# Optimization experiments

Measured on AMD Instinct MI355X. Metric: run time of the kernel, lower is better.

## Reference

```python
import jax, jax.numpy as jnp
import numpy as np

N_CHUNKS = 4 * 28  # hardcoded 112 chunks in the original; chunk sizes are equal when N % 112 == 0


def setup_inputs() -> dict:
    key = jax.random.key(0)
    k1, k2, k3 = jax.random.split(key, 3)
    b, d, h, w = 8, 512, 28, 28  # N = b*h*w = 6272, divisible by 112
    x = jax.random.normal(k1, (b, d, h, w), dtype=jnp.float32)
    p_mu = jax.random.normal(k2, (b * h * w, d), dtype=jnp.float32)
    p_logvar = jax.random.normal(k3, (b * h * w, d), dtype=jnp.float32)
    return {"x": x, "p_mu": p_mu, "p_logvar": p_logvar}


def _club_loss(x, p_mu, p_logvar):
    # (b, d, h, w) -> (N, d) with N = b*h*w
    b, d, h, w = x.shape
    flat_x = jnp.transpose(x, (0, 2, 3, 1)).reshape(-1, d)  # (N, d)

    inv_ev = jnp.exp(-p_logvar)  # (N, d)

    # positive[i] = -0.5 * sum_d (x_i - mu_i)^2 / exp(logvar_i)
    positive = -0.5 * jnp.sum(jnp.square(flat_x - p_mu) * inv_ev, axis=-1)  # (N,)

    # negative[i] = -0.5 * mean_j sum_d (x_j - mu_i)^2 / exp(logvar_i)
    # Expand the square so the j-contraction becomes GEMMs (no (N,N,d) intermediate):
    #   D[i,j] = <x_j^2, inv_ev_i> - 2 <x_j, mu_i * inv_ev_i> + <mu_i^2, inv_ev_i>
    x2 = jnp.square(flat_x)                                   # (N, d)
    term_x2 = jnp.einsum('id,jd->ij', inv_ev, x2)             # (N_i, N_j)
    term_cross = jnp.einsum('id,jd->ij', p_mu * inv_ev, flat_x)
    term_mu2 = jnp.sum(jnp.square(p_mu) * inv_ev, axis=-1, keepdims=True)  # (N_i, 1)
    D = term_x2 - 2.0 * term_cross + term_mu2                 # (N_i, N_j)
    negative = -0.5 * jnp.mean(D, axis=1)                     # (N,)

    # Original averages each of the 112 equal-size chunks then averages the
    # chunk means, which equals the global mean for equal chunk sizes.
    return jnp.mean(positive - negative)


def reference(x, p_mu, p_logvar):
    return _club_loss(x, p_mu, p_logvar)
```

## Files before the change

### kernel.cpp

```cpp
#include <hip/hip_runtime.h>


#define Dd   512
#define HWs  784
#define Nn   6272
#define LSx  260
#define NBLK 392


__global__ __launch_bounds__(256) void club_all(
    const float* __restrict__ x, const float* __restrict__ p_mu,
    const float* __restrict__ p_lv, float* __restrict__ ws,
    float* __restrict__ out)
{
    __shared__ __align__(16) float smem[2 * 16 * LSx];
    __shared__ float sbuf[16];
    __shared__ int lastFlag;

    const int t   = threadIdx.x;
    const int j   = blockIdx.x;
    const int b   = j / 49;
    const int ht  = j % 49;
    const int hw0 = ht * 16;
    const int r0  = b * HWs + hw0;
    const int rep = j & 7;

    const int dx = t >> 2, g = t & 3;
    const float* xb0 = x + ((size_t)(b * Dd + dx) * HWs + hw0 + 4 * g);
    const float4 A0 = *(const float4*)(xb0);
    const float4 A1 = *(const float4*)(xb0 +  64 * HWs);
    const float4 A2 = *(const float4*)(xb0 + 128 * HWs);
    const float4 A3 = *(const float4*)(xb0 + 192 * HWs);
    const float* xb1 = xb0 + 256 * HWs;
    const float4 B0 = *(const float4*)(xb1);
    const float4 B1 = *(const float4*)(xb1 +  64 * HWs);
    const float4 B2 = *(const float4*)(xb1 + 128 * HWs);
    const float4 B3 = *(const float4*)(xb1 + 192 * HWs);

    const size_t mb0 = (size_t)(r0 + (t >> 6)) * Dd + 4 * (t & 63);
    const float4 M00 = *(const float4*)(p_mu + mb0);
    const float4 M01 = *(const float4*)(p_mu + mb0 + 2048);
    const float4 M02 = *(const float4*)(p_mu + mb0 + 4096);
    const float4 M03 = *(const float4*)(p_mu + mb0 + 6144);
    const float4 L00 = *(const float4*)(p_lv + mb0);
    const float4 L01 = *(const float4*)(p_lv + mb0 + 2048);
    const float4 L02 = *(const float4*)(p_lv + mb0 + 4096);
    const float4 L03 = *(const float4*)(p_lv + mb0 + 6144);

#define XST(V, HALF, K) do {                                           \
        const int c_ = dx + 64 * (K);                                  \
        float* s_ = smem + (HALF) * 16 * LSx + (4 * g) * LSx + c_;     \
        s_[0 * LSx] = (V).x; s_[1 * LSx] = (V).y;                      \
        s_[2 * LSx] = (V).z; s_[3 * LSx] = (V).w;                      \
    } while (0)
    XST(A0, 0, 0); XST(A1, 0, 1); XST(A2, 0, 2); XST(A3, 0, 3);
    XST(B0, 1, 0); XST(B1, 1, 1); XST(B2, 1, 2); XST(B3, 1, 3);
#undef XST

    const size_t mb1 = mb0 + 256;
    const float4 M10 = *(const float4*)(p_mu + mb1);
    const float4 M11 = *(const float4*)(p_mu + mb1 + 2048);
    const float4 M12 = *(const float4*)(p_mu + mb1 + 4096);
    const float4 M13 = *(const float4*)(p_mu + mb1 + 6144);
    const float4 L10 = *(const float4*)(p_lv + mb1);
    const float4 L11 = *(const float4*)(p_lv + mb1 + 2048);
    const float4 L12 = *(const float4*)(p_lv + mb1 + 4096);
    const float4 L13 = *(const float4*)(p_lv + mb1 + 6144);

    __syncthreads();

    const int cc = 4 * (t & 63);
    const int rb = t >> 6;
    float4 aI0 = {0,0,0,0}, aM0 = {0,0,0,0}, sX0 = {0,0,0,0}, s20 = {0,0,0,0};
    float4 aI1 = {0,0,0,0}, aM1 = {0,0,0,0}, sX1 = {0,0,0,0}, s21 = {0,0,0,0};
    float aP = 0.f, aM2 = 0.f;

#define ACC1(XV, MU, LV, F, AI, AM, SX, S2) do {                       \
        const float iev = __expf(-(LV).F);                             \
        const float dd  = (XV).F - (MU).F;                             \
        aP += dd * dd * iev;                                           \
        (AI).F += iev;                                                 \
        const float mi = (MU).F * iev;                                 \
        (AM).F += mi; aM2 += (MU).F * mi;                              \
        (SX).F += (XV).F; (S2).F += (XV).F * (XV).F;                   \
    } while (0)
#define ACCROW(HALF, K, MU, LV, AI, AM, SX, S2) do {                   \
        const float4 xv = *(const float4*)&smem[(HALF)*16*LSx + (rb + 4*(K))*LSx + cc]; \
        ACC1(xv, MU, LV, x, AI, AM, SX, S2);                           \
        ACC1(xv, MU, LV, y, AI, AM, SX, S2);                           \
        ACC1(xv, MU, LV, z, AI, AM, SX, S2);                           \
        ACC1(xv, MU, LV, w, AI, AM, SX, S2);                           \
    } while (0)
    ACCROW(0, 0, M00, L00, aI0, aM0, sX0, s20);
    ACCROW(0, 1, M01, L01, aI0, aM0, sX0, s20);
    ACCROW(0, 2, M02, L02, aI0, aM0, sX0, s20);
    ACCROW(0, 3, M03, L03, aI0, aM0, sX0, s20);
    ACCROW(1, 0, M10, L10, aI1, aM1, sX1, s21);
    ACCROW(1, 1, M11, L11, aI1, aM1, sX1, s21);
    ACCROW(1, 2, M12, L12, aI1, aM1, sX1, s21);
    ACCROW(1, 3, M13, L13, aI1, aM1, sX1, s21);
#undef ACCROW
#undef ACC1

    float4* red4 = (float4*)smem;
    float4 rI0, rM0, rX0, r20, rI1, rM1, rX1, r21;
#define COLRED(SRC, DST) do {                                          \
        __syncthreads();                                               \
        red4[t] = (SRC);                                               \
        __syncthreads();                                               \
        if (t < 128) { float4 o = red4[t + 128];                       \
            red4[t].x += o.x; red4[t].y += o.y;                        \
            red4[t].z += o.z; red4[t].w += o.w; }                      \
        __syncthreads();                                               \
        if (t < 64) { float4 a = red4[t], o = red4[t + 64];            \
            (DST).x = a.x + o.x; (DST).y = a.y + o.y;                  \
            (DST).z = a.z + o.z; (DST).w = a.w + o.w; }                \
    } while (0)
    COLRED(aI0, rI0); COLRED(aM0, rM0); COLRED(sX0, rX0); COLRED(s20, r20);
    COLRED(aI1, rI1); COLRED(aM1, rM1); COLRED(sX1, rX1); COLRED(s21, r21);
#undef COLRED

#pragma unroll
    for (int off = 32; off > 0; off >>= 1) {
        aP  += __shfl_down(aP,  off);
        aM2 += __shfl_down(aM2, off);
    }
    __syncthreads();
    if ((t & 63) == 0) { sbuf[t >> 6] = aP; sbuf[8 + (t >> 6)] = aM2; }
    __syncthreads();

    if (t < 64) {
#define ATOM4(OFF, C, V) do {                                          \
        float* p_ = ws + (OFF) + rep * Dd + (C);                       \
        atomicAdd(p_ + 0, (V).x); atomicAdd(p_ + 1, (V).y);            \
        atomicAdd(p_ + 2, (V).z); atomicAdd(p_ + 3, (V).w);            \
    } while (0)
        ATOM4(0,     4 * t,       rI0); ATOM4(0,     256 + 4 * t, rI1);
        ATOM4(4096,  4 * t,       rM0); ATOM4(4096,  256 + 4 * t, rM1);
        ATOM4(8192,  4 * t,       rX0); ATOM4(8192,  256 + 4 * t, rX1);
        ATOM4(12288, 4 * t,       r20); ATOM4(12288, 256 + 4 * t, r21);
#undef ATOM4
    }
    if (t == 0) {
        double* wd = (double*)((char*)ws + 65536);
        atomicAdd(wd + rep,     (double)(sbuf[0] + sbuf[1] + sbuf[2] + sbuf[3]));
        atomicAdd(wd + 8 + rep, (double)(sbuf[8] + sbuf[9] + sbuf[10] + sbuf[11]));
    }

    if (t == 0) {
        __threadfence();
        unsigned* ctr = (unsigned*)((char*)ws + 65664);
        lastFlag = (atomicAdd(ctr, 1u) == NBLK - 1);
    }
    __syncthreads();
    if (!lastFlag) return;

    __threadfence();
    double* redd = (double*)smem;
    double dc = 0.0;
#pragma unroll
    for (int half = 0; half < 2; ++half) {
        const int c = t + 256 * half;
        double sI = 0.0, sM = 0.0, sX = 0.0, s2 = 0.0;
#pragma unroll
        for (int r = 0; r < 8; ++r) {
            sI += (double)__hip_atomic_load(ws +         r * Dd + c, __ATOMIC_RELAXED, __HIP_MEMORY_SCOPE_AGENT);
            sM += (double)__hip_atomic_load(ws +  4096 + r * Dd + c, __ATOMIC_RELAXED, __HIP_MEMORY_SCOPE_AGENT);
            sX += (double)__hip_atomic_load(ws +  8192 + r * Dd + c, __ATOMIC_RELAXED, __HIP_MEMORY_SCOPE_AGENT);
            s2 += (double)__hip_atomic_load(ws + 12288 + r * Dd + c, __ATOMIC_RELAXED, __HIP_MEMORY_SCOPE_AGENT);
        }
        dc += s2 * sI - 2.0 * sX * sM;
    }
    redd[t] = dc; __syncthreads();
    for (int s = 128; s > 0; s >>= 1) {
        if (t < s) redd[t] += redd[t + s];
        __syncthreads();
    }
    if (t == 0) {
        double* wd = (double*)((char*)ws + 65536);
        double P = 0.0, M2 = 0.0;
#pragma unroll
        for (int r = 0; r < 8; ++r) {
            P  += __hip_atomic_load(wd + r,     __ATOMIC_RELAXED, __HIP_MEMORY_SCOPE_AGENT);
            M2 += __hip_atomic_load(wd + 8 + r, __ATOMIC_RELAXED, __HIP_MEMORY_SCOPE_AGENT);
        }
        const double sumD = redd[0] + (double)Nn * M2;
        out[0] = (float)((-0.5 / (double)Nn) * P
                       + (0.5 / ((double)Nn * (double)Nn)) * sumD);
    }
}

extern "C" void kernel_launch(void* const* d_in, const int* in_sizes, int n_in,
                              void* d_out, int out_size, void* d_ws, size_t ws_size,
                              hipStream_t stream) {
    const float* x    = (const float*)d_in[0];
    const float* p_mu = (const float*)d_in[1];
    const float* p_lv = (const float*)d_in[2];
    float* ws = (float*)d_ws;

    hipMemsetAsync(d_ws, 0, 65668, stream);
    club_all<<<NBLK, 256, 0, stream>>>(x, p_mu, p_lv, ws, (float*)d_out);
}
```

Before: 102.6 us.

## Assign one channel per thread and drop shared-memory transpose and column reductions

Each block now covers 28 spatial positions of one 256-channel half, and each thread owns one channel. The thread reads x along hw with float4 loads and reads mu and logvar with strided per-row loads. This removes the LDS transpose staging and the eight multi-sync column reductions, and each thread issues its own atomics, so there are 448 blocks instead of 392. In exchange, the mu and logvar reads become scalar loads coalesced across threads rather than float4 loads, and more float atomics hit the workspace.

```diff
diff --git a/kernel.cpp b/kernel.cpp
--- a/kernel.cpp
+++ b/kernel.cpp
@@ -4,8 +4,7 @@
 #define Dd   512
 #define HWs  784
 #define Nn   6272
-#define LSx  260
-#define NBLK 392
+#define NBLK 448
 
 
 __global__ __launch_bounds__(256) void club_all(
@@ -13,134 +12,59 @@
     const float* __restrict__ p_lv, float* __restrict__ ws,
     float* __restrict__ out)
 {
-    __shared__ __align__(16) float smem[2 * 16 * LSx];
     __shared__ float sbuf[16];
     __shared__ int lastFlag;
+    __shared__ double redd[256];
 
-    const int t   = threadIdx.x;
-    const int j   = blockIdx.x;
-    const int b   = j / 49;
-    const int ht  = j % 49;
-    const int hw0 = ht * 16;
-    const int r0  = b * HWs + hw0;
-    const int rep = j & 7;
+    const int t     = threadIdx.x;
+    const int blk   = blockIdx.x;
+    const int b     = blk / 56;
+    const int rem   = blk % 56;
+    const int half  = rem & 1;
+    const int chunk = rem >> 1;
+    const int hw0   = chunk * 28;
+    const int c     = 256 * half + t;
+    const int r0    = b * HWs + hw0;
+    const int rep   = blk & 7;
 
-    const int dx = t >> 2, g = t & 3;
-    const float* xb0 = x + ((size_t)(b * Dd + dx) * HWs + hw0 + 4 * g);
-    const float4 A0 = *(const float4*)(xb0);
-    const float4 A1 = *(const float4*)(xb0 +  64 * HWs);
-    const float4 A2 = *(const float4*)(xb0 + 128 * HWs);
-    const float4 A3 = *(const float4*)(xb0 + 192 * HWs);
-    const float* xb1 = xb0 + 256 * HWs;
-    const float4 B0 = *(const float4*)(xb1);
-    const float4 B1 = *(const float4*)(xb1 +  64 * HWs);
-    const float4 B2 = *(const float4*)(xb1 + 128 * HWs);
-    const float4 B3 = *(const float4*)(xb1 + 192 * HWs);
+    const float* xr = x + ((size_t)(b * Dd + c) * HWs + hw0);
+    const float* mp = p_mu + (size_t)r0 * Dd + c;
+    const float* lp = p_lv + (size_t)r0 * Dd + c;
 
-    const size_t mb0 = (size_t)(r0 + (t >> 6)) * Dd + 4 * (t & 63);
-    const float4 M00 = *(const float4*)(p_mu + mb0);
-    const float4 M01 = *(const float4*)(p_mu + mb0 + 2048);
-    const float4 M02 = *(const float4*)(p_mu + mb0 + 4096);
-    const float4 M03 = *(const float4*)(p_mu + mb0 + 6144);
-    const float4 L00 = *(const float4*)(p_lv + mb0);
-    const float4 L01 = *(const float4*)(p_lv + mb0 + 2048);
-    const float4 L02 = *(const float4*)(p_lv + mb0 + 4096);
-    const float4 L03 = *(const float4*)(p_lv + mb0 + 6144);
+    float sI = 0.f, sM = 0.f, sX = 0.f, sX2 = 0.f, aP = 0.f, aM2 = 0.f;
 
-#define XST(V, HALF, K) do {                                           \
-        const int c_ = dx + 64 * (K);                                  \
-        float* s_ = smem + (HALF) * 16 * LSx + (4 * g) * LSx + c_;     \
-        s_[0 * LSx] = (V).x; s_[1 * LSx] = (V).y;                      \
-        s_[2 * LSx] = (V).z; s_[3 * LSx] = (V).w;                      \
+#pragma unroll
+    for (int k = 0; k < 7; ++k) {
+        const float4 xq = *(const float4*)(xr + 4 * k);
+        const float xv0 = xq.x, xv1 = xq.y, xv2 = xq.z, xv3 = xq.w;
+#define STEP(J, XV) do {                                               \
+        const size_t ro = (size_t)(4 * k + (J)) * Dd;                  \
+        const float mu = mp[ro];                                       \
+        const float lv = lp[ro];                                       \
+        const float iev = __expf(-lv);                                 \
+        const float dd = (XV) - mu;                                    \
+        aP += dd * dd * iev;                                           \
+        sI += iev;                                                     \
+        const float mi = mu * iev;                                     \
+        sM += mi; aM2 += mu * mi;                                      \
+        sX += (XV); sX2 += (XV) * (XV);                                \
     } while (0)
-    XST(A0, 0, 0); XST(A1, 0, 1); XST(A2, 0, 2); XST(A3, 0, 3);
-    XST(B0, 1, 0); XST(B1, 1, 1); XST(B2, 1, 2); XST(B3, 1, 3);
-#undef XST
-
-    const size_t mb1 = mb0 + 256;
-    const float4 M10 = *(const float4*)(p_mu + mb1);
-    const float4 M11 = *(const float4*)(p_mu + mb1 + 2048);
-    const float4 M12 = *(const float4*)(p_mu + mb1 + 4096);
-    const float4 M13 = *(const float4*)(p_mu + mb1 + 6144);
-    const float4 L10 = *(const float4*)(p_lv + mb1);
-    const float4 L11 = *(const float4*)(p_lv + mb1 + 2048);
-    const float4 L12 = *(const float4*)(p_lv + mb1 + 4096);
-    const float4 L13 = *(const float4*)(p_lv + mb1 + 6144);
-
-    __syncthreads();
-
-    const int cc = 4 * (t & 63);
-    const int rb = t >> 6;
-    float4 aI0 = {0,0,0,0}, aM0 = {0,0,0,0}, sX0 = {0,0,0,0}, s20 = {0,0,0,0};
-    float4 aI1 = {0,0,0,0}, aM1 = {0,0,0,0}, sX1 = {0,0,0,0}, s21 = {0,0,0,0};
-    float aP = 0.f, aM2 = 0.f;
-
-#define ACC1(XV, MU, LV, F, AI, AM, SX, S2) do {                       \
-        const float iev = __expf(-(LV).F);                             \
-        const float dd  = (XV).F - (MU).F;                             \
-        aP += dd * dd * iev;                                           \
-        (AI).F += iev;                                                 \
-        const float mi = (MU).F * iev;                                 \
-        (AM).F += mi; aM2 += (MU).F * mi;                              \
-        (SX).F += (XV).F; (S2).F += (XV).F * (XV).F;                   \
-    } while (0)
-#define ACCROW(HALF, K, MU, LV, AI, AM, SX, S2) do {                   \
-        const float4 xv = *(const float4*)&smem[(HALF)*16*LSx + (rb + 4*(K))*LSx + cc]; \
-        ACC1(xv, MU, LV, x, AI, AM, SX, S2);                           \
-        ACC1(xv, MU, LV, y, AI, AM, SX, S2);                           \
-        ACC1(xv, MU, LV, z, AI, AM, SX, S2);                           \
-        ACC1(xv, MU, LV, w, AI, AM, SX, S2);                           \
-    } while (0)
-    ACCROW(0, 0, M00, L00, aI0, aM0, sX0, s20);
-    ACCROW(0, 1, M01, L01, aI0, aM0, sX0, s20);
-    ACCROW(0, 2, M02, L02, aI0, aM0, sX0, s20);
-    ACCROW(0, 3, M03, L03, aI0, aM0, sX0, s20);
-    ACCROW(1, 0, M10, L10, aI1, aM1, sX1, s21);
-    ACCROW(1, 1, M11, L11, aI1, aM1, sX1, s21);
-    ACCROW(1, 2, M12, L12, aI1, aM1, sX1, s21);
-    ACCROW(1, 3, M13, L13, aI1, aM1, sX1, s21);
-#undef ACCROW
-#undef ACC1
-
-    float4* red4 = (float4*)smem;
-    float4 rI0, rM0, rX0, r20, rI1, rM1, rX1, r21;
-#define COLRED(SRC, DST) do {                                          \
-        __syncthreads();                                               \
-        red4[t] = (SRC);                                               \
-        __syncthreads();                                               \
-        if (t < 128) { float4 o = red4[t + 128];                       \
-            red4[t].x += o.x; red4[t].y += o.y;                        \
-            red4[t].z += o.z; red4[t].w += o.w; }                      \
-        __syncthreads();                                               \
-        if (t < 64) { float4 a = red4[t], o = red4[t + 64];            \
-            (DST).x = a.x + o.x; (DST).y = a.y + o.y;                  \
-            (DST).z = a.z + o.z; (DST).w = a.w + o.w; }                \
-    } while (0)
-    COLRED(aI0, rI0); COLRED(aM0, rM0); COLRED(sX0, rX0); COLRED(s20, r20);
-    COLRED(aI1, rI1); COLRED(aM1, rM1); COLRED(sX1, rX1); COLRED(s21, r21);
-#undef COLRED
+        STEP(0, xv0); STEP(1, xv1); STEP(2, xv2); STEP(3, xv3);
+#undef STEP
+    }
 
 #pragma unroll
     for (int off = 32; off > 0; off >>= 1) {
         aP  += __shfl_down(aP,  off);
         aM2 += __shfl_down(aM2, off);
     }
-    __syncthreads();
     if ((t & 63) == 0) { sbuf[t >> 6] = aP; sbuf[8 + (t >> 6)] = aM2; }
     __syncthreads();
 
-    if (t < 64) {
-#define ATOM4(OFF, C, V) do {                                          \
-        float* p_ = ws + (OFF) + rep * Dd + (C);                       \
-        atomicAdd(p_ + 0, (V).x); atomicAdd(p_ + 1, (V).y);            \
-        atomicAdd(p_ + 2, (V).z); atomicAdd(p_ + 3, (V).w);            \
-    } while (0)
-        ATOM4(0,     4 * t,       rI0); ATOM4(0,     256 + 4 * t, rI1);
-        ATOM4(4096,  4 * t,       rM0); ATOM4(4096,  256 + 4 * t, rM1);
-        ATOM4(8192,  4 * t,       rX0); ATOM4(8192,  256 + 4 * t, rX1);
-        ATOM4(12288, 4 * t,       r20); ATOM4(12288, 256 + 4 * t, r21);
-#undef ATOM4
-    }
+    atomicAdd(&ws[         rep * Dd + c], sI);
+    atomicAdd(&ws[ 4096 + rep * Dd + c], sM);
+    atomicAdd(&ws[ 8192 + rep * Dd + c], sX);
+    atomicAdd(&ws[12288 + rep * Dd + c], sX2);
     if (t == 0) {
         double* wd = (double*)((char*)ws + 65536);
         atomicAdd(wd + rep,     (double)(sbuf[0] + sbuf[1] + sbuf[2] + sbuf[3]));
@@ -156,20 +80,19 @@
     if (!lastFlag) return;
 
     __threadfence();
-    double* redd = (double*)smem;
     double dc = 0.0;
 #pragma unroll
-    for (int half = 0; half < 2; ++half) {
-        const int c = t + 256 * half;
-        double sI = 0.0, sM = 0.0, sX = 0.0, s2 = 0.0;
+    for (int hh = 0; hh < 2; ++hh) {
+        const int cc = t + 256 * hh;
+        double vI = 0.0, vM = 0.0, vX = 0.0, v2 = 0.0;
 #pragma unroll
         for (int r = 0; r < 8; ++r) {
-            sI += (double)__hip_atomic_load(ws +         r * Dd + c, __ATOMIC_RELAXED, __HIP_MEMORY_SCOPE_AGENT);
-            sM += (double)__hip_atomic_load(ws +  4096 + r * Dd + c, __ATOMIC_RELAXED, __HIP_MEMORY_SCOPE_AGENT);
-            sX += (double)__hip_atomic_load(ws +  8192 + r * Dd + c, __ATOMIC_RELAXED, __HIP_MEMORY_SCOPE_AGENT);
-            s2 += (double)__hip_atomic_load(ws + 12288 + r * Dd + c, __ATOMIC_RELAXED, __HIP_MEMORY_SCOPE_AGENT);
+            vI += (double)__hip_atomic_load(ws +         r * Dd + cc, __ATOMIC_RELAXED, __HIP_MEMORY_SCOPE_AGENT);
+            vM += (double)__hip_atomic_load(ws +  4096 + r * Dd + cc, __ATOMIC_RELAXED, __HIP_MEMORY_SCOPE_AGENT);
+            vX += (double)__hip_atomic_load(ws +  8192 + r * Dd + cc, __ATOMIC_RELAXED, __HIP_MEMORY_SCOPE_AGENT);
+            v2 += (double)__hip_atomic_load(ws + 12288 + r * Dd + cc, __ATOMIC_RELAXED, __HIP_MEMORY_SCOPE_AGENT);
         }
-        dc += s2 * sI - 2.0 * sX * sM;
+        dc += v2 * vI - 2.0 * vX * vM;
     }
     redd[t] = dc; __syncthreads();
     for (int s = 128; s > 0; s >>= 1) {
```

Measured after the change: 103.7 us. Within noise of the previous version (+1.1%).
